# Performance work log

Hardware: AMD Instinct MI355X
Metric: run time of the kernel (lower is better)

Reference implementation:

```python
import jax, jax.numpy as jnp
import numpy as np

B, S, D, H = 1, 2048, 4096, 32
HD = D // H  # 128


def _rope_params(seq_len, head_dim, base=10000.0):
    inv_freq = 1.0 / (base ** (np.arange(0, head_dim, 2, dtype=np.float64) / head_dim))
    ang = np.outer(np.arange(seq_len, dtype=np.float64), inv_freq)      # [S, HD/2]
    ang = np.concatenate([ang, ang], axis=-1)                            # [S, HD]
    return jnp.asarray(np.cos(ang), jnp.float32), jnp.asarray(np.sin(ang), jnp.float32)


def _apply_rope(x, cos, sin):
    # x: [B, H, S, HD]; cos/sin: [S, HD]
    half = x.shape[-1] // 2
    x1, x2 = x[..., :half], x[..., half:]
    rotated = jnp.concatenate([-x2, x1], axis=-1)
    return x * cos[None, None] + rotated * sin[None, None]


def setup_inputs() -> dict:
    key = jax.random.key(0)
    ks = jax.random.split(key, 6)
    w_scale = 1.0 / np.sqrt(D)
    X = jax.random.normal(ks[0], (B, S, D), jnp.float32)
    Wq = jax.random.normal(ks[1], (D, D), jnp.float32) * w_scale
    Wk = jax.random.normal(ks[2], (D, D), jnp.float32) * w_scale
    Wv = jax.random.normal(ks[3], (D, D), jnp.float32) * w_scale
    Wo = jax.random.normal(ks[4], (D, D), jnp.float32) * w_scale
    bo = jax.random.normal(ks[5], (D,), jnp.float32) * 0.01
    cos, sin = _rope_params(S, HD)
    return {"X": X, "Wq": Wq, "Wk": Wk, "Wv": Wv, "Wo": Wo, "bo": bo, "cos": cos, "sin": sin}


def reference(X, Wq, Wk, Wv, Wo, bo, cos, sin):
    b, s, d = X.shape
    # nn.Linear: y = x @ W.T
    def split_heads(y):
        return y.reshape(b, s, H, HD).transpose(0, 2, 1, 3)  # [B,H,S,HD]
    q = split_heads(X @ Wq.T)
    k = split_heads(X @ Wk.T)
    v = split_heads(X @ Wv.T)
    q = _apply_rope(q, cos, sin)
    k = _apply_rope(k, cos, sin)
    scores = jnp.einsum('bhqd,bhkd->bhqk', q, k) / np.sqrt(HD).astype(np.float32)
    causal = jnp.tril(jnp.ones((s, s), bool))
    scores = jnp.where(causal[None, None], scores, -jnp.inf)
    attn = jax.nn.softmax(scores, axis=-1)
    out = jnp.einsum('bhqk,bhkd->bhqd', attn, v)  # [B,H,S,HD]
    out = out.transpose(0, 2, 1, 3).reshape(b, s, d)
    return out @ Wo.T + bo
```

## Files before the change

kernel.cpp:

```cpp
#include <hip/hip_runtime.h>

typedef unsigned short u16;
typedef __attribute__((ext_vector_type(8))) short s16x8;
typedef __attribute__((ext_vector_type(4))) float f32x4;

__device__ __forceinline__ u16 f2bf(float f) {
  unsigned u = __float_as_uint(f);
  u += 0x7fffu + ((u >> 16) & 1u);
  return (u16)(u >> 16);
}
__device__ __forceinline__ float bf2f(u16 h) {
  return __uint_as_float(((unsigned)h) << 16);
}
__device__ __forceinline__ unsigned pk2(float lo, float hi) {
  return ((__float_as_uint(hi) + 0x8000u) & 0xffff0000u) |
         ((__float_as_uint(lo) + 0x8000u) >> 16);
}

typedef __attribute__((address_space(1))) const void gvoid_t;
typedef __attribute__((address_space(3))) void lvoid_t;
__device__ __forceinline__ void gload_lds16(const void* g, void* l) {
  __builtin_amdgcn_global_load_lds((gvoid_t*)g, (lvoid_t*)l, 16, 0, 0);
}

__global__ void cvt_f32_bf16(const float* __restrict__ in, u16* __restrict__ out, int n) {
  int i = (blockIdx.x * 256 + threadIdx.x) * 4;
  if (i >= n) return;
  float4 v = *(const float4*)(in + i);
  ushort4 o;
  o.x = f2bf(v.x); o.y = f2bf(v.y); o.z = f2bf(v.z); o.w = f2bf(v.w);
  *(ushort4*)(out + i) = o;
}

template<typename OutT, bool BIAS>
__global__ __launch_bounds__(256) void gemm_bt3(
    const u16* __restrict__ A, const u16* __restrict__ Bm,
    OutT* __restrict__ C, const float* __restrict__ bias,
    int M, int N, int K)
{
  __shared__ u16 As[3][128 * 32];
  __shared__ u16 Bs[3][128 * 32];

  const int t = threadIdx.x;
  const int lane = t & 63, wid = t >> 6;
  const int wm = wid >> 1, wn = wid & 1;
  const int lr = lane & 15, lk = lane >> 4;

  const int wg = blockIdx.x;
  const int xcd = wg & 7, j = wg >> 3;
  const int m0 = (j & 15) * 128;
  const int n0 = ((xcd << 2) | (j >> 4)) * 128;

  const int nt = K >> 5;

  f32x4 acc[4][4] = {};

#define STAGE3(KT)                                                             \
  {                                                                            \
    const int bu_ = (KT) % 3;                                                  \
    const int k0_ = (KT) << 5;                                                 \
    _Pragma("unroll")                                                          \
    for (int it = 0; it < 2; ++it) {                                           \
      int id = it * 256 + t;                                                   \
      int r = id >> 2, c0 = id & 3;                                            \
      int cs = (c0 ^ ((r >> 1) & 3)) << 3;                                     \
      gload_lds16(A + (size_t)(m0 + r) * K + k0_ + cs, &As[bu_][id * 8]);      \
      gload_lds16(Bm + (size_t)(n0 + r) * K + k0_ + cs, &Bs[bu_][id * 8]);     \
    }                                                                          \
  }

  STAGE3(0);
  STAGE3(1);
  asm volatile("s_waitcnt vmcnt(4)" ::: "memory");
  __builtin_amdgcn_s_barrier();

  for (int kt = 0; kt < nt; ++kt) {
    const int bu = kt % 3;
    if (kt + 2 < nt) STAGE3(kt + 2);

    s16x8 af[4], bf[4];
#pragma unroll
    for (int i = 0; i < 4; ++i) {
      int ra = wm * 64 + i * 16 + lr;
      af[i] = *(const s16x8*)&As[bu][ra * 32 + ((lk ^ ((ra >> 1) & 3)) << 3)];
      int rb = wn * 64 + i * 16 + lr;
      bf[i] = *(const s16x8*)&Bs[bu][rb * 32 + ((lk ^ ((rb >> 1) & 3)) << 3)];
    }
    __builtin_amdgcn_s_setprio(1);
#pragma unroll
    for (int i = 0; i < 4; ++i)
#pragma unroll
      for (int jn = 0; jn < 4; ++jn)
        acc[i][jn] = __builtin_amdgcn_mfma_f32_16x16x32_bf16(af[i], bf[jn], acc[i][jn], 0, 0, 0);
    __builtin_amdgcn_s_setprio(0);

    asm volatile("s_waitcnt lgkmcnt(0)" ::: "memory");
    if (kt + 2 < nt)       { asm volatile("s_waitcnt vmcnt(4)" ::: "memory"); }
    else if (kt + 2 == nt) { asm volatile("s_waitcnt vmcnt(0)" ::: "memory"); }
    if (kt + 1 < nt) __builtin_amdgcn_s_barrier();
  }
#undef STAGE3

#pragma unroll
  for (int i = 0; i < 4; ++i) {
    int row_b = m0 + wm * 64 + i * 16 + lk * 4;
#pragma unroll
    for (int jn = 0; jn < 4; ++jn) {
      int col = n0 + wn * 64 + jn * 16 + lr;
      float bv = BIAS ? bias[col] : 0.f;
#pragma unroll
      for (int r = 0; r < 4; ++r) {
        float v = acc[i][jn][r] + bv;
        size_t off = (size_t)(row_b + r) * N + col;
        if constexpr (sizeof(OutT) == 2) ((u16*)C)[off] = f2bf(v);
        else                             ((float*)C)[off] = v;
      }
    }
  }
}

__global__ __launch_bounds__(256) void gemm_qkv(
    const u16* __restrict__ A, const u16* __restrict__ Bstk,
    u16* __restrict__ Qb, u16* __restrict__ Kb, u16* __restrict__ Vb,
    int M, int K)
{
  __shared__ u16 As[3][128 * 32];
  __shared__ u16 Bs[3][128 * 32];

  const int t = threadIdx.x;
  const int lane = t & 63, wid = t >> 6;
  const int wm = wid >> 1, wn = wid & 1;
  const int lr = lane & 15, lk = lane >> 4;

  const int wg = blockIdx.x;
  const int xcd = wg & 7, j = wg >> 3;
  const int m0 = (j & 15) * 128;
  const int n0 = (xcd * 12 + (j >> 4)) * 128;

  const int nt = K >> 5;

  f32x4 acc[4][4] = {};

#define STAGEQ(KT)                                                             \
  {                                                                            \
    const int bu_ = (KT) % 3;                                                  \
    const int k0_ = (KT) << 5;                                                 \
    _Pragma("unroll")                                                          \
    for (int it = 0; it < 2; ++it) {                                           \
      int id = it * 256 + t;                                                   \
      int r = id >> 2, c0 = id & 3;                                            \
      int cs = (c0 ^ ((r >> 1) & 3)) << 3;                                     \
      gload_lds16(A + (size_t)(m0 + r) * K + k0_ + cs, &As[bu_][id * 8]);      \
      gload_lds16(Bstk + (size_t)(n0 + r) * K + k0_ + cs, &Bs[bu_][id * 8]);   \
    }                                                                          \
  }

  STAGEQ(0);
  STAGEQ(1);
  asm volatile("s_waitcnt vmcnt(4)" ::: "memory");
  __builtin_amdgcn_s_barrier();

  for (int kt = 0; kt < nt; ++kt) {
    const int bu = kt % 3;
    if (kt + 2 < nt) STAGEQ(kt + 2);

    s16x8 af[4], bf[4];
#pragma unroll
    for (int i = 0; i < 4; ++i) {
      int ra = wm * 64 + i * 16 + lr;
      af[i] = *(const s16x8*)&As[bu][ra * 32 + ((lk ^ ((ra >> 1) & 3)) << 3)];
      int rb = wn * 64 + i * 16 + lr;
      bf[i] = *(const s16x8*)&Bs[bu][rb * 32 + ((lk ^ ((rb >> 1) & 3)) << 3)];
    }
    __builtin_amdgcn_s_setprio(1);
#pragma unroll
    for (int i = 0; i < 4; ++i)
#pragma unroll
      for (int jn = 0; jn < 4; ++jn)
        acc[i][jn] = __builtin_amdgcn_mfma_f32_16x16x32_bf16(af[i], bf[jn], acc[i][jn], 0, 0, 0);
    __builtin_amdgcn_s_setprio(0);

    asm volatile("s_waitcnt lgkmcnt(0)" ::: "memory");
    if (kt + 2 < nt)       { asm volatile("s_waitcnt vmcnt(4)" ::: "memory"); }
    else if (kt + 2 == nt) { asm volatile("s_waitcnt vmcnt(0)" ::: "memory"); }
    if (kt + 1 < nt) __builtin_amdgcn_s_barrier();
  }
#undef STAGEQ

  u16* Cp; int nb;
  if (n0 < 4096)      { Cp = Qb; nb = n0; }
  else if (n0 < 8192) { Cp = Kb; nb = n0 - 4096; }
  else                { Cp = Vb; nb = n0 - 8192; }

#pragma unroll
  for (int i = 0; i < 4; ++i) {
    int row_b = m0 + wm * 64 + i * 16 + lk * 4;
#pragma unroll
    for (int jn = 0; jn < 4; ++jn) {
      int col = nb + wn * 64 + jn * 16 + lr;
#pragma unroll
      for (int r = 0; r < 4; ++r)
        Cp[(size_t)(row_b + r) * 4096 + col] = f2bf(acc[i][jn][r]);
    }
  }
}

__global__ void rope_qk(u16* __restrict__ Q, u16* __restrict__ Kt,
                        const float* __restrict__ cosp, const float* __restrict__ sinp) {
  int i = blockIdx.x * 256 + threadIdx.x;
  int d = i & 63;
  int h = (i >> 6) & 31;
  int s = i >> 11;
  float c = cosp[s * 128 + d], sn = sinp[s * 128 + d];
  size_t base = (size_t)s * 4096 + h * 128 + d;
  float q1 = bf2f(Q[base]), q2 = bf2f(Q[base + 64]);
  Q[base]      = f2bf(q1 * c - q2 * sn);
  Q[base + 64] = f2bf(q2 * c + q1 * sn);
  float k1 = bf2f(Kt[base]), k2 = bf2f(Kt[base + 64]);
  Kt[base]      = f2bf(k1 * c - k2 * sn);
  Kt[base + 64] = f2bf(k2 * c + k1 * sn);
}

__global__ __launch_bounds__(256) void flash_attn(
    const u16* __restrict__ Q, const u16* __restrict__ Kg, const u16* __restrict__ Vg,
    u16* __restrict__ Ctx)
{
  const int D = 4096;
  __shared__ u16 Ks[2][64 * 128];
  __shared__ u16 Vt[128 * 64];

  const int t = threadIdx.x, lane = t & 63, wid = t >> 6;
  const int lr = lane & 15, lk = lane >> 4;

  const int wg = blockIdx.x;
  const int xcd = wg & 7, j = wg >> 3;
  const int bx = 31 - (j >> 2);
  const int h = xcd * 4 + (j & 3);
  const int q0 = bx * 64;
  const int qw0 = q0 + wid * 16;

  s16x8 qf[4];
#pragma unroll
  for (int kc = 0; kc < 4; ++kc)
    qf[kc] = *(const s16x8*)(Q + (size_t)(qw0 + lr) * D + h * 128 + kc * 32 + lk * 8);

  f32x4 o[8] = {};
  float m_s = -1e30f, l_s = 0.f;

  const int ntiles = bx + 1;
  const float scale2 = 0.12751779f;

  const int ch = t & 15, kv4 = (t >> 4) * 4;

  {
#pragma unroll
    for (int it = 0; it < 4; ++it) {
      int id = it * 256 + t;
      int kv = id >> 4, c0 = id & 15;
      gload_lds16(Kg + (size_t)kv * D + h * 128 + ((c0 ^ (kv & 7)) << 3), &Ks[0][id * 8]);
    }
    const u16* src = Vg + (size_t)kv4 * D + h * 128 + ch * 8;
    s16x8 v0 = *(const s16x8*)src;
    s16x8 v1 = *(const s16x8*)(src + D);
    s16x8 v2 = *(const s16x8*)(src + 2 * D);
    s16x8 v3 = *(const s16x8*)(src + 3 * D);
#pragma unroll
    for (int jj = 0; jj < 8; ++jj) {
      int d = ch * 8 + jj;
      int sw = ((ch ^ jj) & 7) << 3;
      *(unsigned*)&Vt[d * 64 + ((kv4)     ^ sw)] = (unsigned)(u16)v0[jj] | ((unsigned)(u16)v1[jj] << 16);
      *(unsigned*)&Vt[d * 64 + ((kv4 + 2) ^ sw)] = (unsigned)(u16)v2[jj] | ((unsigned)(u16)v3[jj] << 16);
    }
  }

  for (int kt = 0; kt < ntiles; ++kt) {
    const int b = kt & 1;
    const int kv0 = kt * 64;
    __syncthreads();

    s16x8 v0, v1, v2, v3;
    const bool pf = (kt + 1 < ntiles);
    if (pf) {
      const u16* src = Vg + (size_t)(kv0 + 64 + kv4) * D + h * 128 + ch * 8;
      v0 = *(const s16x8*)src;
      v1 = *(const s16x8*)(src + D);
      v2 = *(const s16x8*)(src + 2 * D);
      v3 = *(const s16x8*)(src + 3 * D);
#pragma unroll
      for (int it = 0; it < 4; ++it) {
        int id = it * 256 + t;
        int kv = id >> 4, c0 = id & 15;
        gload_lds16(Kg + (size_t)(kv0 + 64 + kv) * D + h * 128 + ((c0 ^ (kv & 7)) << 3),
                    &Ks[b ^ 1][id * 8]);
      }
    }

    if (kv0 <= qw0 + 15) {
      const bool masked = (kv0 + 63 > qw0);

      f32x4 st[4] = {};
      __builtin_amdgcn_s_setprio(1);
#pragma unroll
      for (int nt = 0; nt < 4; ++nt) {
        int kv = nt * 16 + lr;
        int sw = kv & 7;
#pragma unroll
        for (int kc = 0; kc < 4; ++kc) {
          s16x8 kf = *(const s16x8*)&Ks[b][kv * 128 + (((4 * kc + lk) ^ sw) << 3)];
          st[nt] = __builtin_amdgcn_mfma_f32_16x16x32_bf16(kf, qf[kc], st[nt], 0, 0, 0);
        }
      }
      __builtin_amdgcn_s_setprio(0);

      float pm = -1e30f;
#pragma unroll
      for (int nt = 0; nt < 4; ++nt)
#pragma unroll
        for (int r = 0; r < 4; ++r) {
          float sv = st[nt][r] * scale2;
          if (masked && (kv0 + nt * 16 + lk * 4 + r > qw0 + lr)) sv = -1e30f;
          st[nt][r] = sv;
          pm = fmaxf(pm, sv);
        }
      pm = fmaxf(pm, __shfl_xor(pm, 16));
      pm = fmaxf(pm, __shfl_xor(pm, 32));

      if (__any(pm > m_s + 8.f)) {
        float mn = fmaxf(m_s, pm);
        float al = __builtin_amdgcn_exp2f(m_s - mn);
        m_s = mn; l_s *= al;
        float aq0 = __shfl(al, (lane & 48) | (lk * 4 + 0));
        float aq1 = __shfl(al, (lane & 48) | (lk * 4 + 1));
        float aq2 = __shfl(al, (lane & 48) | (lk * 4 + 2));
        float aq3 = __shfl(al, (lane & 48) | (lk * 4 + 3));
#pragma unroll
        for (int nb = 0; nb < 8; ++nb) {
          o[nb][0] *= aq0; o[nb][1] *= aq1; o[nb][2] *= aq2; o[nb][3] *= aq3;
        }
      }

      float ps = 0.f;
#pragma unroll
      for (int nt = 0; nt < 4; ++nt)
#pragma unroll
        for (int r = 0; r < 4; ++r) {
          float pv = __builtin_amdgcn_exp2f(st[nt][r] - m_s);
          st[nt][r] = pv;
          ps += pv;
        }
      ps += __shfl_xor(ps, 16);
      ps += __shfl_xor(ps, 32);
      l_s += ps;

      unsigned pkv[4][2];
#pragma unroll
      for (int nt = 0; nt < 4; ++nt) {
        pkv[nt][0] = pk2(st[nt][0], st[nt][1]);
        pkv[nt][1] = pk2(st[nt][2], st[nt][3]);
      }

      const int srcA = lr | (((lk & 1) * 2) << 4);
      const int srcB = srcA + 16;
      const bool sel = (lk >> 1) != 0;
      s16x8 pa[2];
#pragma unroll
      for (int ks = 0; ks < 2; ++ks) {
        int a0 = __shfl((int)pkv[ks * 2][0], srcA);
        int b0 = __shfl((int)pkv[ks * 2 + 1][0], srcA);
        int a1 = __shfl((int)pkv[ks * 2][1], srcA);
        int b1 = __shfl((int)pkv[ks * 2 + 1][1], srcA);
        int a2 = __shfl((int)pkv[ks * 2][0], srcB);
        int b2 = __shfl((int)pkv[ks * 2 + 1][0], srcB);
        int a3 = __shfl((int)pkv[ks * 2][1], srcB);
        int b3 = __shfl((int)pkv[ks * 2 + 1][1], srcB);
        int4 w = { sel ? b0 : a0, sel ? b1 : a1, sel ? b2 : a2, sel ? b3 : a3 };
        pa[ks] = *(s16x8*)&w;
      }

      __builtin_amdgcn_s_setprio(1);
#pragma unroll
      for (int ks = 0; ks < 2; ++ks) {
#pragma unroll
        for (int nb = 0; nb < 8; ++nb) {
          int d = nb * 16 + lr;
          int g = (((d >> 3) ^ d) & 7) << 3;
          s16x8 vf = *(const s16x8*)&Vt[d * 64 + ((ks * 32 + lk * 8) ^ g)];
          o[nb] = __builtin_amdgcn_mfma_f32_16x16x32_bf16(pa[ks], vf, o[nb], 0, 0, 0);
        }
      }
      __builtin_amdgcn_s_setprio(0);
    }

    if (pf) {
      __builtin_amdgcn_s_barrier();
#pragma unroll
      for (int jj = 0; jj < 8; ++jj) {
        int d = ch * 8 + jj;
        int sw = ((ch ^ jj) & 7) << 3;
        *(unsigned*)&Vt[d * 64 + ((kv4)     ^ sw)] = (unsigned)(u16)v0[jj] | ((unsigned)(u16)v1[jj] << 16);
        *(unsigned*)&Vt[d * 64 + ((kv4 + 2) ^ sw)] = (unsigned)(u16)v2[jj] | ((unsigned)(u16)v3[jj] << 16);
      }
    }
  }

  float linv = 1.f / l_s;
  float i0 = __shfl(linv, (lane & 48) | (lk * 4 + 0));
  float i1 = __shfl(linv, (lane & 48) | (lk * 4 + 1));
  float i2 = __shfl(linv, (lane & 48) | (lk * 4 + 2));
  float i3 = __shfl(linv, (lane & 48) | (lk * 4 + 3));
#pragma unroll
  for (int nb = 0; nb < 8; ++nb) {
    int d = h * 128 + nb * 16 + lr;
    Ctx[(size_t)(qw0 + lk * 4 + 0) * D + d] = f2bf(o[nb][0] * i0);
    Ctx[(size_t)(qw0 + lk * 4 + 1) * D + d] = f2bf(o[nb][1] * i1);
    Ctx[(size_t)(qw0 + lk * 4 + 2) * D + d] = f2bf(o[nb][2] * i2);
    Ctx[(size_t)(qw0 + lk * 4 + 3) * D + d] = f2bf(o[nb][3] * i3);
  }
}

extern "C" void kernel_launch(void* const* d_in, const int* in_sizes, int n_in,
                              void* d_out, int out_size, void* d_ws, size_t ws_size,
                              hipStream_t stream) {
  const int S = 2048, D = 4096, H = 32;
  const size_t SD = (size_t)S * D, DD = (size_t)D * D;

  const float* X  = (const float*)d_in[0];
  const float* Wq = (const float*)d_in[1];
  const float* Wk = (const float*)d_in[2];
  const float* Wv = (const float*)d_in[3];
  const float* Wo = (const float*)d_in[4];
  const float* bo = (const float*)d_in[5];
  const float* cs = (const float*)d_in[6];
  const float* sn = (const float*)d_in[7];

  dim3 blk(256);
  dim3 g3(512);
  dim3 b3(256);

  const size_t need_fused = (3 * DD + 4 * SD) * sizeof(u16);

  if (ws_size >= need_fused) {
    u16* WB3 = (u16*)d_ws;
    u16* Xb  = WB3 + 3 * DD;
    u16* Qb  = Xb + SD;
    u16* Kb  = Qb + SD;
    u16* Vb  = Kb + SD;

    cvt_f32_bf16<<<(int)(SD / 1024), blk, 0, stream>>>(X, Xb, (int)SD);
    cvt_f32_bf16<<<(int)(DD / 1024), blk, 0, stream>>>(Wq, WB3, (int)DD);
    cvt_f32_bf16<<<(int)(DD / 1024), blk, 0, stream>>>(Wk, WB3 + DD, (int)DD);
    cvt_f32_bf16<<<(int)(DD / 1024), blk, 0, stream>>>(Wv, WB3 + 2 * DD, (int)DD);

    gemm_qkv<<<dim3(1536), b3, 0, stream>>>(Xb, WB3, Qb, Kb, Vb, S, D);

    rope_qk<<<(S * H * 64) / 256, blk, 0, stream>>>(Qb, Kb, cs, sn);
    flash_attn<<<dim3(1024), dim3(256), 0, stream>>>(Qb, Kb, Vb, Xb );

    cvt_f32_bf16<<<(int)(DD / 1024), blk, 0, stream>>>(Wo, WB3, (int)DD);
    gemm_bt3<float, true><<<g3, b3, 0, stream>>>(Xb, WB3, (float*)d_out, bo, S, D, D);
  } else {
    u16* WB = (u16*)d_ws;
    u16* Xb = WB + DD;
    u16* Qb = Xb + SD;
    u16* Kb = Qb + SD;
    u16* Vb = Kb + SD;

    cvt_f32_bf16<<<(int)(SD / 1024), blk, 0, stream>>>(X, Xb, (int)SD);
    cvt_f32_bf16<<<(int)(DD / 1024), blk, 0, stream>>>(Wq, WB, (int)DD);
    gemm_bt3<u16, false><<<g3, b3, 0, stream>>>(Xb, WB, Qb, nullptr, S, D, D);
    cvt_f32_bf16<<<(int)(DD / 1024), blk, 0, stream>>>(Wk, WB, (int)DD);
    gemm_bt3<u16, false><<<g3, b3, 0, stream>>>(Xb, WB, Kb, nullptr, S, D, D);
    cvt_f32_bf16<<<(int)(DD / 1024), blk, 0, stream>>>(Wv, WB, (int)DD);
    gemm_bt3<u16, false><<<g3, b3, 0, stream>>>(Xb, WB, Vb, nullptr, S, D, D);

    rope_qk<<<(S * H * 64) / 256, blk, 0, stream>>>(Qb, Kb, cs, sn);
    flash_attn<<<dim3(1024), dim3(256), 0, stream>>>(Qb, Kb, Vb, Xb );

    cvt_f32_bf16<<<(int)(DD / 1024), blk, 0, stream>>>(Wo, WB, (int)DD);
    gemm_bt3<float, true><<<g3, b3, 0, stream>>>(Xb, WB, (float*)d_out, bo, S, D, D);
  }
}
```

Before: 493.1 us.

## Switch GEMMs to 32x32x16 MFMA and fuse input conversions into one kernel

```diff
diff --git a/kernel.cpp b/kernel.cpp
--- a/kernel.cpp
+++ b/kernel.cpp
@@ -3,6 +3,7 @@
 typedef unsigned short u16;
 typedef __attribute__((ext_vector_type(8))) short s16x8;
 typedef __attribute__((ext_vector_type(4))) float f32x4;
+typedef __attribute__((ext_vector_type(16))) float f32x16;
 
 __device__ __forceinline__ u16 f2bf(float f) {
   unsigned u = __float_as_uint(f);
@@ -30,6 +31,26 @@
   ushort4 o;
   o.x = f2bf(v.x); o.y = f2bf(v.y); o.z = f2bf(v.z); o.w = f2bf(v.w);
   *(ushort4*)(out + i) = o;
+}
+
+__global__ void cvt4(const float* __restrict__ X,
+                     const float* __restrict__ Wq, const float* __restrict__ Wk,
+                     const float* __restrict__ Wv,
+                     u16* __restrict__ Xb, u16* __restrict__ WB3) {
+  long i = ((long)blockIdx.x * 256 + threadIdx.x) * 4;
+  const float* src; u16* dst; long off;
+  if (i < (1L << 23)) { src = X; dst = Xb; off = i; }
+  else {
+    long k = i - (1L << 23);
+    int w = (int)(k >> 24);
+    off = k & ((1L << 24) - 1);
+    src = (w == 0) ? Wq : (w == 1) ? Wk : Wv;
+    dst = WB3 + ((size_t)w << 24);
+  }
+  float4 v = *(const float4*)(src + off);
+  ushort4 o;
+  o.x = f2bf(v.x); o.y = f2bf(v.y); o.z = f2bf(v.z); o.w = f2bf(v.w);
+  *(ushort4*)(dst + off) = o;
 }
 
 template<typename OutT, bool BIAS>
@@ -44,7 +65,7 @@
   const int t = threadIdx.x;
   const int lane = t & 63, wid = t >> 6;
   const int wm = wid >> 1, wn = wid & 1;
-  const int lr = lane & 15, lk = lane >> 4;
+  const int l31 = lane & 31, l5 = lane >> 5;
 
   const int wg = blockIdx.x;
   const int xcd = wg & 7, j = wg >> 3;
@@ -53,7 +74,7 @@
 
   const int nt = K >> 5;
 
-  f32x4 acc[4][4] = {};
+  f32x16 acc[2][2] = {};
 
 #define STAGE3(KT)                                                             \
   {                                                                            \
@@ -78,20 +99,26 @@
     const int bu = kt % 3;
     if (kt + 2 < nt) STAGE3(kt + 2);
 
-    s16x8 af[4], bf[4];
-#pragma unroll
-    for (int i = 0; i < 4; ++i) {
-      int ra = wm * 64 + i * 16 + lr;
-      af[i] = *(const s16x8*)&As[bu][ra * 32 + ((lk ^ ((ra >> 1) & 3)) << 3)];
-      int rb = wn * 64 + i * 16 + lr;
-      bf[i] = *(const s16x8*)&Bs[bu][rb * 32 + ((lk ^ ((rb >> 1) & 3)) << 3)];
-    }
+    s16x8 af[2][2], bf[2][2];
+#pragma unroll
+    for (int ks = 0; ks < 2; ++ks)
+#pragma unroll
+      for (int mt = 0; mt < 2; ++mt) {
+        int ra = wm * 64 + mt * 32 + l31;
+        int c = ks * 2 + l5;
+        af[ks][mt] = *(const s16x8*)&As[bu][ra * 32 + ((c ^ ((ra >> 1) & 3)) << 3)];
+        int rb = wn * 64 + mt * 32 + l31;
+        bf[ks][mt] = *(const s16x8*)&Bs[bu][rb * 32 + ((c ^ ((rb >> 1) & 3)) << 3)];
+      }
     __builtin_amdgcn_s_setprio(1);
 #pragma unroll
-    for (int i = 0; i < 4; ++i)
-#pragma unroll
-      for (int jn = 0; jn < 4; ++jn)
-        acc[i][jn] = __builtin_amdgcn_mfma_f32_16x16x32_bf16(af[i], bf[jn], acc[i][jn], 0, 0, 0);
+    for (int ks = 0; ks < 2; ++ks)
+#pragma unroll
+      for (int mt = 0; mt < 2; ++mt)
+#pragma unroll
+        for (int ntl = 0; ntl < 2; ++ntl)
+          acc[mt][ntl] = __builtin_amdgcn_mfma_f32_32x32x16_bf16(
+              af[ks][mt], bf[ks][ntl], acc[mt][ntl], 0, 0, 0);
     __builtin_amdgcn_s_setprio(0);
 
     asm volatile("s_waitcnt lgkmcnt(0)" ::: "memory");
@@ -102,21 +129,20 @@
 #undef STAGE3
 
 #pragma unroll
-  for (int i = 0; i < 4; ++i) {
-    int row_b = m0 + wm * 64 + i * 16 + lk * 4;
-#pragma unroll
-    for (int jn = 0; jn < 4; ++jn) {
-      int col = n0 + wn * 64 + jn * 16 + lr;
+  for (int mt = 0; mt < 2; ++mt)
+#pragma unroll
+    for (int ntl = 0; ntl < 2; ++ntl) {
+      int col = n0 + wn * 64 + ntl * 32 + l31;
       float bv = BIAS ? bias[col] : 0.f;
 #pragma unroll
-      for (int r = 0; r < 4; ++r) {
-        float v = acc[i][jn][r] + bv;
-        size_t off = (size_t)(row_b + r) * N + col;
+      for (int reg = 0; reg < 16; ++reg) {
+        int row = m0 + wm * 64 + mt * 32 + 4 * l5 + (reg & 3) + 8 * (reg >> 2);
+        float v = acc[mt][ntl][reg] + bv;
+        size_t off = (size_t)row * N + col;
         if constexpr (sizeof(OutT) == 2) ((u16*)C)[off] = f2bf(v);
         else                             ((float*)C)[off] = v;
       }
     }
-  }
 }
 
 __global__ __launch_bounds__(256) void gemm_qkv(
@@ -130,7 +156,7 @@
   const int t = threadIdx.x;
   const int lane = t & 63, wid = t >> 6;
   const int wm = wid >> 1, wn = wid & 1;
-  const int lr = lane & 15, lk = lane >> 4;
+  const int l31 = lane & 31, l5 = lane >> 5;
 
   const int wg = blockIdx.x;
   const int xcd = wg & 7, j = wg >> 3;
@@ -139,7 +165,7 @@
 
   const int nt = K >> 5;
 
-  f32x4 acc[4][4] = {};
+  f32x16 acc[2][2] = {};
 
 #define STAGEQ(KT)                                                             \
   {                                                                            \
@@ -164,20 +190,26 @@
     const int bu = kt % 3;
     if (kt + 2 < nt) STAGEQ(kt + 2);
 
-    s16x8 af[4], bf[4];
-#pragma unroll
-    for (int i = 0; i < 4; ++i) {
-      int ra = wm * 64 + i * 16 + lr;
-      af[i] = *(const s16x8*)&As[bu][ra * 32 + ((lk ^ ((ra >> 1) & 3)) << 3)];
-      int rb = wn * 64 + i * 16 + lr;
-      bf[i] = *(const s16x8*)&Bs[bu][rb * 32 + ((lk ^ ((rb >> 1) & 3)) << 3)];
-    }
+    s16x8 af[2][2], bf[2][2];
+#pragma unroll
+    for (int ks = 0; ks < 2; ++ks)
+#pragma unroll
+      for (int mt = 0; mt < 2; ++mt) {
+        int ra = wm * 64 + mt * 32 + l31;
+        int c = ks * 2 + l5;
+        af[ks][mt] = *(const s16x8*)&As[bu][ra * 32 + ((c ^ ((ra >> 1) & 3)) << 3)];
+        int rb = wn * 64 + mt * 32 + l31;
+        bf[ks][mt] = *(const s16x8*)&Bs[bu][rb * 32 + ((c ^ ((rb >> 1) & 3)) << 3)];
+      }
     __builtin_amdgcn_s_setprio(1);
 #pragma unroll
-    for (int i = 0; i < 4; ++i)
-#pragma unroll
-      for (int jn = 0; jn < 4; ++jn)
-        acc[i][jn] = __builtin_amdgcn_mfma_f32_16x16x32_bf16(af[i], bf[jn], acc[i][jn], 0, 0, 0);
+    for (int ks = 0; ks < 2; ++ks)
+#pragma unroll
+      for (int mt = 0; mt < 2; ++mt)
+#pragma unroll
+        for (int ntl = 0; ntl < 2; ++ntl)
+          acc[mt][ntl] = __builtin_amdgcn_mfma_f32_32x32x16_bf16(
+              af[ks][mt], bf[ks][ntl], acc[mt][ntl], 0, 0, 0);
     __builtin_amdgcn_s_setprio(0);
 
     asm volatile("s_waitcnt lgkmcnt(0)" ::: "memory");
@@ -193,16 +225,16 @@
   else                { Cp = Vb; nb = n0 - 8192; }
 
 #pragma unroll
-  for (int i = 0; i < 4; ++i) {
-    int row_b = m0 + wm * 64 + i * 16 + lk * 4;
-#pragma unroll
-    for (int jn = 0; jn < 4; ++jn) {
-      int col = nb + wn * 64 + jn * 16 + lr;
-#pragma unroll
-      for (int r = 0; r < 4; ++r)
-        Cp[(size_t)(row_b + r) * 4096 + col] = f2bf(acc[i][jn][r]);
-    }
-  }
+  for (int mt = 0; mt < 2; ++mt)
+#pragma unroll
+    for (int ntl = 0; ntl < 2; ++ntl) {
+      int col = nb + wn * 64 + ntl * 32 + l31;
+#pragma unroll
+      for (int reg = 0; reg < 16; ++reg) {
+        int row = m0 + wm * 64 + mt * 32 + 4 * l5 + (reg & 3) + 8 * (reg >> 2);
+        Cp[(size_t)row * 4096 + col] = f2bf(acc[mt][ntl][reg]);
+      }
+    }
 }
 
 __global__ void rope_qk(u16* __restrict__ Q, u16* __restrict__ Kt,
@@ -446,10 +478,7 @@
     u16* Kb  = Qb + SD;
     u16* Vb  = Kb + SD;
 
-    cvt_f32_bf16<<<(int)(SD / 1024), blk, 0, stream>>>(X, Xb, (int)SD);
-    cvt_f32_bf16<<<(int)(DD / 1024), blk, 0, stream>>>(Wq, WB3, (int)DD);
-    cvt_f32_bf16<<<(int)(DD / 1024), blk, 0, stream>>>(Wk, WB3 + DD, (int)DD);
-    cvt_f32_bf16<<<(int)(DD / 1024), blk, 0, stream>>>(Wv, WB3 + 2 * DD, (int)DD);
+    cvt4<<<(int)((SD + 3 * DD) / 1024), blk, 0, stream>>>(X, Wq, Wk, Wv, Xb, WB3);
 
     gemm_qkv<<<dim3(1536), b3, 0, stream>>>(Xb, WB3, Qb, Kb, Vb, S, D);
 
```

Measured after the change: 523.2 us. 1.06x slower.
